# Kernel optimization log

Measured on AMD Instinct MI355X. Metric: run time of the kernel, lower is better.

## Reference

```python
import jax, jax.numpy as jnp
import numpy as np

MASK_VALUE = 1.0e6   # mask_value default in get_interpolation
N_NH = 3             # nh_inter: number of nearest neighbors kept by topk
POWER = 2            # inverse-distance weighting power
CUTOFF_DIST = 0.01   # cutoff_dist: distances clamped below this value


def setup_inputs() -> dict:
    key = jax.random.key(0)
    k1, k2, k3 = jax.random.split(key, 3)
    b, n_l, l, nh, nv, f = 1, 4096, 16, 1, 4, 1
    nh_sz, nt = 9, 16            # neighbor cells per cell; target points per cell
    n = n_l * l                  # 65536 fine-grid points
    K = nh_sz * l * nh           # 144 candidate source points per cell
    x = jax.random.normal(k1, (b, n, nh, nv, f), dtype=jnp.float32)
    mask = jnp.zeros((b, n, nh, nv), dtype=jnp.float32)  # 0 = valid point
    dist = jax.random.uniform(k2, (b, n_l, nt, K), dtype=jnp.float32)
    nh_idx = jax.random.randint(k3, (n_l, nh_sz), 0, n_l)  # neighbor-cell table
    return {"x": x, "mask": mask, "dist": dist, "nh_idx": nh_idx}


def reference(x, mask, dist, nh_idx):
    b, n, nh, nv, f = x.shape            # f == 1 (required by original gather layout)
    _, n_l, nt, K = dist.shape
    l = n // n_l
    # --- get_nh: group fine points into coarse cells, gather neighbor cells ---
    x_c = x.reshape(b, n_l, l * nh * nv * f)
    m_c = mask.reshape(b, n_l, l * nh * nv)
    x_nh = x_c[:, nh_idx].reshape(b, n_l, K, nv, f)      # (b,n_l,K,nv,f)
    mask_nh = m_c[:, nh_idx].reshape(b, n_l, K, nv)      # (b,n_l,K,nv)
    # --- masked distances broadcast over target points and variables ---
    dist_m = dist[:, :, :, :, None] + mask_nh[:, :, None, :, :] * MASK_VALUE  # (b,n_l,nt,K,nv)
    dist_m = jnp.moveaxis(dist_m, 3, -1)                 # (b,n_l,nt,nv,K)
    # --- top-k smallest distances (irregular topk) ---
    neg_vals, idx = jax.lax.top_k(-dist_m, N_NH)
    dist_vals = -neg_vals                                # (b,n_l,nt,nv,N_NH)
    # --- gather selected neighbor features ---
    xh = jnp.moveaxis(x_nh[..., 0], 2, -1)               # (b,n_l,nv,K)
    xh = jnp.broadcast_to(xh[:, :, None], (b, n_l, nt, nv, K))
    x_g = jnp.take_along_axis(xh, idx, axis=-1)          # (b,n_l,nt,nv,N_NH)
    # --- inverse-distance weights ---
    dv = jnp.maximum(dist_vals, CUTOFF_DIST)
    w = 1.0 / dv ** POWER
    w = w / w.sum(axis=-1, keepdims=True)
    x_inter = (x_g * w).sum(axis=-1)                     # (b,n_l,nt,nv)
    return x_inter.reshape(b, n_l * nt, nv, f)
```

## Files before the change

kernel.cpp:

```cpp
#include <hip/hip_runtime.h>

#define N_L   4096
#define NT    16
#define NV    4
#define NHSZ  9
#define KCAND 144
#define MASKV 1.0e6f
#define CUT   0.01f
#define BIG   3.0e38f

__device__ __forceinline__ bool lex_lt(float da, int ia, float db, int ib) {
    return (da < db) || ((da == db) && (ia < ib));
}

__global__ __launch_bounds__(256) void interp_kernel(
    const float* __restrict__ x,
    const float* __restrict__ mask,
    const float* __restrict__ dist,
    const int*   __restrict__ nh_idx,
    float*       __restrict__ out)
{
    __shared__ int s_cells[4 * NHSZ];
    __shared__ int s_dirty[4];

    const int t    = threadIdx.x;
    const int row0 = blockIdx.x * 64;
    const int c0   = row0 >> 4;

    if (t < 4) s_dirty[t] = 0;
    if (t < 4 * NHSZ) s_cells[t] = nh_idx[c0 * NHSZ + t];
    __syncthreads();

#pragma unroll
    for (int i = 0; i < 9; ++i) {
        int f = t + 256 * i;
        int e = f >> 6;
        int w = f & 63;
        float m = mask[s_cells[e] * 64 + w];
        if (m != 0.0f) atomicOr(&s_dirty[e / 9], 1);
    }
    __syncthreads();

    const int row = row0 + (t >> 2);
    const int sub = t & 3;
    const int lc  = (t >> 2) >> 4;
    const int* cells = &s_cells[lc * NHSZ];

    if (s_dirty[lc] == 0) {
        const float4* dp = (const float4*)(dist + (size_t)row * KCAND);
        float d0 = BIG, d1 = BIG, d2 = BIG;
        int   i0 = 0,   i1 = 0,   i2 = 0;
#pragma unroll
        for (int m = 0; m < 9; ++m) {
            float4 dd = dp[sub + 4 * m];
            const float de[4] = {dd.x, dd.y, dd.z, dd.w};
            const int kb = 4 * sub + 16 * m;
#pragma unroll
            for (int e = 0; e < 4; ++e) {
                float d = de[e];
                int   k = kb + e;
                bool c0_ = d < d0, c1_ = d < d1, c2_ = d < d2;
                d2 = c1_ ? d1 : (c2_ ? d : d2);
                i2 = c1_ ? i1 : (c2_ ? k : i2);
                d1 = c0_ ? d0 : (c1_ ? d : d1);
                i1 = c0_ ? i0 : (c1_ ? k : i1);
                d0 = c0_ ? d  : d0;
                i0 = c0_ ? k  : i0;
            }
        }

#pragma unroll
        for (int mm = 0; mm < 2; ++mm) {
            const int msk = 1 << mm;
            float ed0 = __shfl_xor(d0, msk);
            float ed1 = __shfl_xor(d1, msk);
            float ed2 = __shfl_xor(d2, msk);
            int   ei0 = __shfl_xor(i0, msk);
            int   ei1 = __shfl_xor(i1, msk);
            int   ei2 = __shfl_xor(i2, msk);
            bool cA = lex_lt(d0, i0, ed0, ei0);
            float lo0d = cA ? d0 : ed0;  int lo0i = cA ? i0 : ei0;
            float hi0d = cA ? ed0 : d0;  int hi0i = cA ? ei0 : i0;
            bool cB = lex_lt(d1, i1, ed1, ei1);
            float lo1d = cB ? d1 : ed1;  int lo1i = cB ? i1 : ei1;
            float hi1d = cB ? ed1 : d1;  int hi1i = cB ? ei1 : i1;
            bool cC = lex_lt(d2, i2, ed2, ei2);
            float lo2d = cC ? d2 : ed2;  int lo2i = cC ? i2 : ei2;
            bool cD = lex_lt(hi0d, hi0i, lo1d, lo1i);
            float r1d = cD ? hi0d : lo1d; int r1i = cD ? hi0i : lo1i;
            float t2d = cD ? lo1d : hi0d; int t2i = cD ? lo1i : hi0i;
            bool cE = lex_lt(t2d, t2i, lo2d, lo2i);
            float r2d = cE ? t2d : lo2d;  int r2i = cE ? t2i : lo2i;
            d0 = lo0d; i0 = lo0i;
            d1 = r1d;  i1 = r1i;
            d2 = r2d;  i2 = r2i;
        }

        float v0 = fmaxf(d0, CUT), v1 = fmaxf(d1, CUT), v2 = fmaxf(d2, CUT);
        float w0 = 1.0f / (v0 * v0);
        float w1 = 1.0f / (v1 * v1);
        float w2 = 1.0f / (v2 * v2);
        float inv = 1.0f / (w0 + w1 + w2);
        int j0 = i0 >> 4, p0 = i0 & 15;
        int j1 = i1 >> 4, p1 = i1 & 15;
        int j2 = i2 >> 4, p2 = i2 & 15;
        float xa = x[cells[j0] * 64 + p0 * 4 + sub];
        float xb = x[cells[j1] * 64 + p1 * 4 + sub];
        float xd = x[cells[j2] * 64 + p2 * 4 + sub];
        out[row * 4 + sub] = (xa * w0 + xb * w1 + xd * w2) * inv;
    } else {
        const float* dr = dist + (size_t)row * KCAND;
        float d0 = BIG, d1 = BIG, d2 = BIG;
        int   i0 = 0,   i1 = 0,   i2 = 0;
        for (int k = 0; k < KCAND; ++k) {
            int j = k >> 4, p = k & 15;
            float dm = fmaf(mask[cells[j] * 64 + p * 4 + sub], MASKV, dr[k]);
            bool c0_ = dm < d0, c1_ = dm < d1, c2_ = dm < d2;
            d2 = c1_ ? d1 : (c2_ ? dm : d2);
            i2 = c1_ ? i1 : (c2_ ? k  : i2);
            d1 = c0_ ? d0 : (c1_ ? dm : d1);
            i1 = c0_ ? i0 : (c1_ ? k  : i1);
            d0 = c0_ ? dm : d0;
            i0 = c0_ ? k  : i0;
        }
        float v0 = fmaxf(d0, CUT), v1 = fmaxf(d1, CUT), v2 = fmaxf(d2, CUT);
        float w0 = 1.0f / (v0 * v0);
        float w1 = 1.0f / (v1 * v1);
        float w2 = 1.0f / (v2 * v2);
        float inv = 1.0f / (w0 + w1 + w2);
        float xa = x[cells[i0 >> 4] * 64 + (i0 & 15) * 4 + sub];
        float xb = x[cells[i1 >> 4] * 64 + (i1 & 15) * 4 + sub];
        float xd = x[cells[i2 >> 4] * 64 + (i2 & 15) * 4 + sub];
        out[row * 4 + sub] = (xa * w0 + xb * w1 + xd * w2) * inv;
    }
}

extern "C" void kernel_launch(void* const* d_in, const int* in_sizes, int n_in,
                              void* d_out, int out_size, void* d_ws, size_t ws_size,
                              hipStream_t stream) {
    const float* x      = (const float*)d_in[0];
    const float* mask   = (const float*)d_in[1];
    const float* dist   = (const float*)d_in[2];
    const int*   nh_idx = (const int*)d_in[3];
    float*       out    = (float*)d_out;

    interp_kernel<<<(N_L * NT * 4) / 256, 256, 0, stream>>>(x, mask, dist,
                                                            nh_idx, out);
}
```

Measured before the change: 87.69 us.

## Use 8 threads per row and prefetch distance data before the mask scan

Each block now covers 32 rows instead of 64, with 8 lanes per row scanning the 144 candidates instead of 4, and a third shuffle merge stage to combine the partial top-3 lists. The distance loads are issued before the shared-memory setup and the mask dirty scan, so their latency overlaps that work. Launch bounds ask for 8 blocks per CU. The cost is twice as many blocks, duplicated mask scanning per block, and half the lanes sitting idle in the final gather and in the masked fallback path.

```diff
diff --git a/kernel.cpp b/kernel.cpp
--- a/kernel.cpp
+++ b/kernel.cpp
@@ -13,64 +13,79 @@
     return (da < db) || ((da == db) && (ia < ib));
 }
 
-__global__ __launch_bounds__(256) void interp_kernel(
+__global__ __launch_bounds__(256, 8) void interp_kernel(
     const float* __restrict__ x,
     const float* __restrict__ mask,
     const float* __restrict__ dist,
     const int*   __restrict__ nh_idx,
     float*       __restrict__ out)
 {
-    __shared__ int s_cells[4 * NHSZ];
-    __shared__ int s_dirty[4];
+    __shared__ int s_cells[2 * NHSZ];
+    __shared__ int s_dirty[2];
 
     const int t    = threadIdx.x;
-    const int row0 = blockIdx.x * 64;
+    const int row0 = blockIdx.x * 32;
     const int c0   = row0 >> 4;
+    const int row  = row0 + (t >> 3);
+    const int sub8 = t & 7;
+    const int sub  = t & 3;
+    const int lc   = t >> 7;
 
-    if (t < 4) s_dirty[t] = 0;
-    if (t < 4 * NHSZ) s_cells[t] = nh_idx[c0 * NHSZ + t];
+    const float4* dp = (const float4*)(dist + (size_t)row * KCAND);
+    float4 cA = dp[sub8];
+    float4 cB = dp[sub8 + 8];
+    float4 cC = dp[sub8 + 16];
+    float4 cD = dp[sub8 + 24];
+    float4 cE = dp[32 + (sub8 & 3)];
+
+    if (t < 2) s_dirty[t] = 0;
+    if (t < 2 * NHSZ) s_cells[t] = nh_idx[c0 * NHSZ + t];
     __syncthreads();
 
 #pragma unroll
-    for (int i = 0; i < 9; ++i) {
+    for (int i = 0; i < 5; ++i) {
         int f = t + 256 * i;
-        int e = f >> 6;
-        int w = f & 63;
-        float m = mask[s_cells[e] * 64 + w];
-        if (m != 0.0f) atomicOr(&s_dirty[e / 9], 1);
+        if (f < 2 * NHSZ * 64) {
+            int e = f >> 6;
+            int w = f & 63;
+            float m = mask[s_cells[e] * 64 + w];
+            if (m != 0.0f) atomicOr(&s_dirty[e / NHSZ], 1);
+        }
     }
     __syncthreads();
 
-    const int row = row0 + (t >> 2);
-    const int sub = t & 3;
-    const int lc  = (t >> 2) >> 4;
     const int* cells = &s_cells[lc * NHSZ];
 
     if (s_dirty[lc] == 0) {
-        const float4* dp = (const float4*)(dist + (size_t)row * KCAND);
         float d0 = BIG, d1 = BIG, d2 = BIG;
         int   i0 = 0,   i1 = 0,   i2 = 0;
-#pragma unroll
-        for (int m = 0; m < 9; ++m) {
-            float4 dd = dp[sub + 4 * m];
-            const float de[4] = {dd.x, dd.y, dd.z, dd.w};
-            const int kb = 4 * sub + 16 * m;
-#pragma unroll
-            for (int e = 0; e < 4; ++e) {
-                float d = de[e];
-                int   k = kb + e;
-                bool c0_ = d < d0, c1_ = d < d1, c2_ = d < d2;
-                d2 = c1_ ? d1 : (c2_ ? d : d2);
-                i2 = c1_ ? i1 : (c2_ ? k : i2);
-                d1 = c0_ ? d0 : (c1_ ? d : d1);
-                i1 = c0_ ? i0 : (c1_ ? k : i1);
-                d0 = c0_ ? d  : d0;
-                i0 = c0_ ? k  : i0;
-            }
-        }
+
+#define INS(dv, kv) do {                                                   \
+            float d_ = (dv); int k_ = (kv);                                \
+            bool c0_ = d_ < d0, c1_ = d_ < d1, c2_ = d_ < d2;              \
+            d2 = c1_ ? d1 : (c2_ ? d_ : d2);                               \
+            i2 = c1_ ? i1 : (c2_ ? k_ : i2);                               \
+            d1 = c0_ ? d0 : (c1_ ? d_ : d1);                               \
+            i1 = c0_ ? i0 : (c1_ ? k_ : i1);                               \
+            d0 = c0_ ? d_ : d0;                                            \
+            i0 = c0_ ? k_ : i0;                                            \
+        } while (0)
+#define INS4(c, q) do {                                                    \
+            int kb_ = 4 * (q);                                             \
+            INS((c).x, kb_ + 0); INS((c).y, kb_ + 1);                      \
+            INS((c).z, kb_ + 2); INS((c).w, kb_ + 3);                      \
+        } while (0)
+
+        INS4(cA, sub8);
+        INS4(cB, sub8 + 8);
+        INS4(cC, sub8 + 16);
+        INS4(cD, sub8 + 24);
+        if (sub8 < 4) INS4(cE, 32 + sub8);
+#undef INS4
+#undef INS
 
 #pragma unroll
-        for (int mm = 0; mm < 2; ++mm) {
+        for (int mm = 0; mm < 3; ++mm) {
             const int msk = 1 << mm;
             float ed0 = __shfl_xor(d0, msk);
             float ed1 = __shfl_xor(d1, msk);
@@ -78,60 +93,64 @@
             int   ei0 = __shfl_xor(i0, msk);
             int   ei1 = __shfl_xor(i1, msk);
             int   ei2 = __shfl_xor(i2, msk);
-            bool cA = lex_lt(d0, i0, ed0, ei0);
-            float lo0d = cA ? d0 : ed0;  int lo0i = cA ? i0 : ei0;
-            float hi0d = cA ? ed0 : d0;  int hi0i = cA ? ei0 : i0;
-            bool cB = lex_lt(d1, i1, ed1, ei1);
-            float lo1d = cB ? d1 : ed1;  int lo1i = cB ? i1 : ei1;
-            float hi1d = cB ? ed1 : d1;  int hi1i = cB ? ei1 : i1;
-            bool cC = lex_lt(d2, i2, ed2, ei2);
-            float lo2d = cC ? d2 : ed2;  int lo2i = cC ? i2 : ei2;
-            bool cD = lex_lt(hi0d, hi0i, lo1d, lo1i);
-            float r1d = cD ? hi0d : lo1d; int r1i = cD ? hi0i : lo1i;
-            float t2d = cD ? lo1d : hi0d; int t2i = cD ? lo1i : hi0i;
-            bool cE = lex_lt(t2d, t2i, lo2d, lo2i);
-            float r2d = cE ? t2d : lo2d;  int r2i = cE ? t2i : lo2i;
+            bool cA_ = lex_lt(d0, i0, ed0, ei0);
+            float lo0d = cA_ ? d0 : ed0;  int lo0i = cA_ ? i0 : ei0;
+            float hi0d = cA_ ? ed0 : d0;  int hi0i = cA_ ? ei0 : i0;
+            bool cB_ = lex_lt(d1, i1, ed1, ei1);
+            float lo1d = cB_ ? d1 : ed1;  int lo1i = cB_ ? i1 : ei1;
+            float hi1d = cB_ ? ed1 : d1;  int hi1i = cB_ ? ei1 : i1;
+            bool cC_ = lex_lt(d2, i2, ed2, ei2);
+            float lo2d = cC_ ? d2 : ed2;  int lo2i = cC_ ? i2 : ei2;
+            bool cD_ = lex_lt(hi0d, hi0i, lo1d, lo1i);
+            float r1d = cD_ ? hi0d : lo1d; int r1i = cD_ ? hi0i : lo1i;
+            float t2d = cD_ ? lo1d : hi0d; int t2i = cD_ ? lo1i : hi0i;
+            bool cE_ = lex_lt(t2d, t2i, lo2d, lo2i);
+            float r2d = cE_ ? t2d : lo2d;  int r2i = cE_ ? t2i : lo2i;
             d0 = lo0d; i0 = lo0i;
             d1 = r1d;  i1 = r1i;
             d2 = r2d;  i2 = r2i;
         }
 
-        float v0 = fmaxf(d0, CUT), v1 = fmaxf(d1, CUT), v2 = fmaxf(d2, CUT);
-        float w0 = 1.0f / (v0 * v0);
-        float w1 = 1.0f / (v1 * v1);
-        float w2 = 1.0f / (v2 * v2);
-        float inv = 1.0f / (w0 + w1 + w2);
-        int j0 = i0 >> 4, p0 = i0 & 15;
-        int j1 = i1 >> 4, p1 = i1 & 15;
-        int j2 = i2 >> 4, p2 = i2 & 15;
-        float xa = x[cells[j0] * 64 + p0 * 4 + sub];
-        float xb = x[cells[j1] * 64 + p1 * 4 + sub];
-        float xd = x[cells[j2] * 64 + p2 * 4 + sub];
-        out[row * 4 + sub] = (xa * w0 + xb * w1 + xd * w2) * inv;
+        if (sub8 < 4) {
+            float v0 = fmaxf(d0, CUT), v1 = fmaxf(d1, CUT), v2 = fmaxf(d2, CUT);
+            float w0 = 1.0f / (v0 * v0);
+            float w1 = 1.0f / (v1 * v1);
+            float w2 = 1.0f / (v2 * v2);
+            float inv = 1.0f / (w0 + w1 + w2);
+            int j0 = i0 >> 4, p0 = i0 & 15;
+            int j1 = i1 >> 4, p1 = i1 & 15;
+            int j2 = i2 >> 4, p2 = i2 & 15;
+            float xa = x[cells[j0] * 64 + p0 * 4 + sub];
+            float xb = x[cells[j1] * 64 + p1 * 4 + sub];
+            float xd = x[cells[j2] * 64 + p2 * 4 + sub];
+            out[row * 4 + sub] = (xa * w0 + xb * w1 + xd * w2) * inv;
+        }
     } else {
-        const float* dr = dist + (size_t)row * KCAND;
-        float d0 = BIG, d1 = BIG, d2 = BIG;
-        int   i0 = 0,   i1 = 0,   i2 = 0;
-        for (int k = 0; k < KCAND; ++k) {
-            int j = k >> 4, p = k & 15;
-            float dm = fmaf(mask[cells[j] * 64 + p * 4 + sub], MASKV, dr[k]);
-            bool c0_ = dm < d0, c1_ = dm < d1, c2_ = dm < d2;
-            d2 = c1_ ? d1 : (c2_ ? dm : d2);
-            i2 = c1_ ? i1 : (c2_ ? k  : i2);
-            d1 = c0_ ? d0 : (c1_ ? dm : d1);
-            i1 = c0_ ? i0 : (c1_ ? k  : i1);
-            d0 = c0_ ? dm : d0;
-            i0 = c0_ ? k  : i0;
+        if ((t & 4) == 0) {
+            const float* dr = dist + (size_t)row * KCAND;
+            float d0 = BIG, d1 = BIG, d2 = BIG;
+            int   i0 = 0,   i1 = 0,   i2 = 0;
+            for (int k = 0; k < KCAND; ++k) {
+                int j = k >> 4, p = k & 15;
+                float dm = fmaf(mask[cells[j] * 64 + p * 4 + sub], MASKV, dr[k]);
+                bool c0_ = dm < d0, c1_ = dm < d1, c2_ = dm < d2;
+                d2 = c1_ ? d1 : (c2_ ? dm : d2);
+                i2 = c1_ ? i1 : (c2_ ? k  : i2);
+                d1 = c0_ ? d0 : (c1_ ? dm : d1);
+                i1 = c0_ ? i0 : (c1_ ? k  : i1);
+                d0 = c0_ ? dm : d0;
+                i0 = c0_ ? k  : i0;
+            }
+            float v0 = fmaxf(d0, CUT), v1 = fmaxf(d1, CUT), v2 = fmaxf(d2, CUT);
+            float w0 = 1.0f / (v0 * v0);
+            float w1 = 1.0f / (v1 * v1);
+            float w2 = 1.0f / (v2 * v2);
+            float inv = 1.0f / (w0 + w1 + w2);
+            float xa = x[cells[i0 >> 4] * 64 + (i0 & 15) * 4 + sub];
+            float xb = x[cells[i1 >> 4] * 64 + (i1 & 15) * 4 + sub];
+            float xd = x[cells[i2 >> 4] * 64 + (i2 & 15) * 4 + sub];
+            out[row * 4 + sub] = (xa * w0 + xb * w1 + xd * w2) * inv;
         }
-        float v0 = fmaxf(d0, CUT), v1 = fmaxf(d1, CUT), v2 = fmaxf(d2, CUT);
-        float w0 = 1.0f / (v0 * v0);
-        float w1 = 1.0f / (v1 * v1);
-        float w2 = 1.0f / (v2 * v2);
-        float inv = 1.0f / (w0 + w1 + w2);
-        float xa = x[cells[i0 >> 4] * 64 + (i0 & 15) * 4 + sub];
-        float xb = x[cells[i1 >> 4] * 64 + (i1 & 15) * 4 + sub];
-        float xd = x[cells[i2 >> 4] * 64 + (i2 & 15) * 4 + sub];
-        out[row * 4 + sub] = (xa * w0 + xb * w1 + xd * w2) * inv;
     }
 }
 
@@ -144,6 +163,6 @@
     const int*   nh_idx = (const int*)d_in[3];
     float*       out    = (float*)d_out;
 
-    interp_kernel<<<(N_L * NT * 4) / 256, 256, 0, stream>>>(x, mask, dist,
-                                                            nh_idx, out);
+    interp_kernel<<<(N_L * NT) / 32, 256, 0, stream>>>(x, mask, dist,
+                                                       nh_idx, out);
 }
```

New measurement: 89.39 us. No clear change (+1.9%).
